# Kernel optimization log

Measured on AMD Instinct MI355X. Metric: run time of the kernel, lower is better.

## Reference

```python
import jax, jax.numpy as jnp
import numpy as np
import math

B, N, C = 8, 1024, 256
NUM_HEAD = 4
HEAD_DIM = C // NUM_HEAD
K_NN = 5
SAMPLE_RATIO = 0.25
CLUSTER_NUM = max(math.ceil(N * SAMPLE_RATIO), 1)
EPS = 1e-6


def cluster_dpc_knn(x, cluster_num, k):
    # DPC-KNN clustering (faithful to TCFormer's cluster_dpc_knn, run under no_grad in torch)
    b, n, c = x.shape
    sq = jnp.sum(x * x, axis=-1)
    d2 = sq[:, :, None] + sq[:, None, :] - 2.0 * jnp.einsum('bic,bjc->bij', x, x)
    dist = jnp.sqrt(jnp.maximum(d2, 0.0)) / jnp.sqrt(jnp.asarray(c, x.dtype))  # (b,n,n)
    # k smallest distances per token (includes self, dist 0)
    neg_near, _ = jax.lax.top_k(-dist, k)
    dist_nearest = -neg_near
    density = jnp.exp(-jnp.mean(dist_nearest ** 2, axis=-1))  # (b,n)
    # deterministic tiny noise for tie-breaking (torch adds rand*1e-6)
    density = density + jax.random.uniform(jax.random.key(42), density.shape, dtype=density.dtype) * 1e-6
    mask = (density[:, None, :] > density[:, :, None]).astype(x.dtype)
    dist_max = jnp.max(dist.reshape(b, -1), axis=-1)[:, None, None]
    d_ind = jnp.min(dist * mask + dist_max * (1.0 - mask), axis=-1)  # distance indicator
    score = d_ind * density
    _, index_down = jax.lax.top_k(score, cluster_num)  # (b,cluster_num) cluster centers
    dist_c = jnp.take_along_axis(dist, index_down[:, :, None], axis=1)  # (b,cn,n)
    idx_cluster = jnp.argmin(dist_c, axis=1)  # (b,n)
    # ensure each center maps to its own cluster id
    bidx = jnp.arange(b)[:, None]
    idx_cluster = idx_cluster.at[bidx, index_down].set(jnp.broadcast_to(jnp.arange(cluster_num)[None, :], (b, cluster_num)))
    return idx_cluster


def setup_inputs() -> dict:
    key = jax.random.key(0)
    ks = jax.random.split(key, 6)
    w_scale = 1.0 / jnp.sqrt(jnp.asarray(C, jnp.float32))
    x_token = jax.random.normal(ks[0], (B, N, C), dtype=jnp.float32)
    Wq = jax.random.normal(ks[1], (C, C), dtype=jnp.float32) * w_scale
    Wk = jax.random.normal(ks[2], (C, C), dtype=jnp.float32) * w_scale
    Wv = jax.random.normal(ks[3], (C, C), dtype=jnp.float32) * w_scale
    Wp = jax.random.normal(ks[4], (C, C), dtype=jnp.float32) * w_scale
    bp = jax.random.normal(ks[5], (C,), dtype=jnp.float32) * 0.01
    return {"x_token": x_token, "Wq": Wq, "Wk": Wk, "Wv": Wv, "Wp": Wp, "bp": bp}


def reference(x_token, Wq, Wk, Wv, Wp, bp):
    b, n, c = x_token.shape
    scale = HEAD_DIM ** -0.5
    idx_cluster = cluster_dpc_knn(x_token, CLUSTER_NUM, K_NN)  # (b,n) int
    q = (x_token @ Wq.T).reshape(b, n, NUM_HEAD, HEAD_DIM).transpose(0, 2, 1, 3)
    k = (x_token @ Wk.T).reshape(b, n, NUM_HEAD, HEAD_DIM).transpose(0, 2, 1, 3)
    v = (x_token @ Wv.T).reshape(b, n, NUM_HEAD, HEAD_DIM).transpose(0, 2, 1, 3)
    scores = jnp.einsum('bhid,bhjd->bhij', q, k) * scale  # (b,h,n,n)
    # scatter into (b,cluster_num,n,c) + sum over clusters == mask scores by same-cluster
    same = (idx_cluster[:, :, None] == idx_cluster[:, None, :])[:, None, :, :]
    attn = jnp.where(same, scores, 0.0)
    # original: masked_fill(attn == 0, -1e9) then exp in float32
    attn = jnp.where(attn == 0.0, -1e9, attn)
    attn = jnp.exp(attn.astype(jnp.float32))
    attn = (attn + EPS / n) / (jnp.sum(attn, axis=-1, keepdims=True) + EPS)
    out = jnp.einsum('bhij,bhjd->bhid', attn, v).transpose(0, 2, 1, 3).reshape(b, n, c)
    return out @ Wp.T + bp
```

## Files before the change

### kernel.cpp

```cpp
#include <hip/hip_runtime.h>
#include <math.h>

#define B_ 8
#define N_ 1024
#define C_ 256
#define H_ 4
#define D_ 64
#define CN_ 256
#define EPS_ 1e-6f

__device__ __forceinline__ unsigned rotl32(unsigned x, int r){ return (x<<r)|(x>>(32-r)); }

__device__ float tf_noise(unsigned gid){
  unsigned c0 = (gid >= 4096u) ? gid - 4096u : gid;
  unsigned c1 = c0 + 4096u;
  const unsigned k0 = 0u, k1 = 42u;
  const unsigned ks2 = k0 ^ k1 ^ 0x1BD11BDAu;
  unsigned x0 = c0 + k0, x1 = c1 + k1;
  const int R0[4] = {13,15,26,6};
  const int R1[4] = {17,29,16,24};
  #pragma unroll
  for (int i=0;i<4;i++){ x0 += x1; x1 = rotl32(x1,R0[i]); x1 ^= x0; }
  x0 += k1; x1 += ks2 + 1u;
  #pragma unroll
  for (int i=0;i<4;i++){ x0 += x1; x1 = rotl32(x1,R1[i]); x1 ^= x0; }
  x0 += ks2; x1 += k0 + 2u;
  #pragma unroll
  for (int i=0;i<4;i++){ x0 += x1; x1 = rotl32(x1,R0[i]); x1 ^= x0; }
  x0 += k0; x1 += k1 + 3u;
  #pragma unroll
  for (int i=0;i<4;i++){ x0 += x1; x1 = rotl32(x1,R1[i]); x1 ^= x0; }
  x0 += k1; x1 += ks2 + 4u;
  #pragma unroll
  for (int i=0;i<4;i++){ x0 += x1; x1 = rotl32(x1,R0[i]); x1 ^= x0; }
  x0 += ks2; x1 += k0 + 5u;
  unsigned bits = (gid >= 4096u) ? x1 : x0;
  return __uint_as_float(0x3F800000u | (bits >> 9)) - 1.0f;
}

__global__ __launch_bounds__(256) void k_sq(const float* __restrict__ x, float* __restrict__ sq){
  int row = blockIdx.x * 4 + (threadIdx.x >> 6);
  int l = threadIdx.x & 63;
  const float* p = x + (size_t)row * C_;
  float s = 0.f;
  #pragma unroll
  for (int t=0;t<4;t++){ float v = p[l + 64*t]; s += v*v; }
  #pragma unroll
  for (int m=32;m;m>>=1) s += __shfl_xor(s, m);
  if (l==0) sq[row] = s;
}

#define STAGE64(PA, PB)                                                        \
  _Pragma("unroll")                                                            \
  for (int f=0; f<4; f++){                                                     \
    int e = f*64 + t; int row = e >> 2, kq = e & 3;                            \
    float4 a = *(const float4*)(PA + (size_t)row*C_ + k0 + kq*4);              \
    float4 bq = *(const float4*)(PB + (size_t)row*C_ + k0 + kq*4);             \
    As[kq*4+0][row]=a.x;  As[kq*4+1][row]=a.y;                                 \
    As[kq*4+2][row]=a.z;  As[kq*4+3][row]=a.w;                                 \
    Bs[kq*4+0][row]=bq.x; Bs[kq*4+1][row]=bq.y;                                \
    Bs[kq*4+2][row]=bq.z; Bs[kq*4+3][row]=bq.w;                                \
  }

#define INNER64                                                                \
  _Pragma("unroll")                                                            \
  for (int kk=0;kk<16;kk++){                                                   \
    float4 a0 = *(const float4*)&As[kk][ty*4];                                 \
    float4 a1 = *(const float4*)&As[kk][32+ty*4];                              \
    float4 b0 = *(const float4*)&Bs[kk][tx*4];                                 \
    float4 b1 = *(const float4*)&Bs[kk][32+tx*4];                              \
    float av[8]={a0.x,a0.y,a0.z,a0.w,a1.x,a1.y,a1.z,a1.w};                     \
    float bv[8]={b0.x,b0.y,b0.z,b0.w,b1.x,b1.y,b1.z,b1.w};                     \
    _Pragma("unroll")                                                          \
    for (int r=0;r<8;r++)                                                      \
      _Pragma("unroll")                                                        \
      for (int c=0;c<8;c++) acc[r][c] += av[r]*bv[c];                          \
  }

__global__ __launch_bounds__(64) void k_dist3(const float* __restrict__ x, const float* __restrict__ sq,
                                              float* __restrict__ dist){
  int b = blockIdx.y;
  int p = blockIdx.x;
  int bi = 0, rem = p;
  while (rem >= 16 - bi){ rem -= 16 - bi; bi++; }
  int bj = bi + rem;
  const float* xb = x + (size_t)b*N_*C_;
  const float* pa = xb + (size_t)(bi*64)*C_;
  const float* pb = xb + (size_t)(bj*64)*C_;
  __shared__ float As[16][68];
  __shared__ float Bs[16][68];
  int t = threadIdx.x;
  int tx = t & 7, ty = t >> 3;
  float acc[8][8] = {};
  for (int k0=0; k0<C_; k0+=16){
    STAGE64(pa, pb)
    __syncthreads();
    INNER64
    __syncthreads();
  }
  float sqj[8];
  #pragma unroll
  for (int cc=0;cc<2;cc++)
    #pragma unroll
    for (int c=0;c<4;c++) sqj[cc*4+c] = sq[b*N_ + bj*64 + cc*32 + tx*4 + c];
  float o[8][8];
  #pragma unroll
  for (int rr=0;rr<2;rr++){
    #pragma unroll
    for (int r=0;r<4;r++){
      int i = bi*64 + rr*32 + ty*4 + r;
      float si = sq[b*N_ + i];
      #pragma unroll
      for (int cc=0;cc<2;cc++)
        #pragma unroll
        for (int c=0;c<4;c++){
          float d2 = si + sqj[cc*4+c] - 2.f*acc[rr*4+r][cc*4+c];
          o[rr*4+r][cc*4+c] = sqrtf(fmaxf(d2, 0.f)) * 0.0625f;
        }
    }
  }
  float* dbase = dist + (size_t)b*N_*N_;
  #pragma unroll
  for (int rr=0;rr<2;rr++)
    #pragma unroll
    for (int r=0;r<4;r++){
      int i = bi*64 + rr*32 + ty*4 + r;
      #pragma unroll
      for (int cc=0;cc<2;cc++){
        int j0 = bj*64 + cc*32 + tx*4;
        *(float4*)(dbase + (size_t)i*N_ + j0) =
          make_float4(o[rr*4+r][cc*4+0], o[rr*4+r][cc*4+1], o[rr*4+r][cc*4+2], o[rr*4+r][cc*4+3]);
      }
    }
  if (bi != bj){
    #pragma unroll
    for (int cc=0;cc<2;cc++)
      #pragma unroll
      for (int c=0;c<4;c++){
        int j = bj*64 + cc*32 + tx*4 + c;
        #pragma unroll
        for (int rr=0;rr<2;rr++){
          int i0 = bi*64 + rr*32 + ty*4;
          *(float4*)(dbase + (size_t)j*N_ + i0) =
            make_float4(o[rr*4+0][cc*4+c], o[rr*4+1][cc*4+c], o[rr*4+2][cc*4+c], o[rr*4+3][cc*4+c]);
        }
      }
  }
}

__global__ __launch_bounds__(64) void k_gemm3(const float* __restrict__ X,
    const float* __restrict__ W0, const float* __restrict__ W1, const float* __restrict__ W2,
    const float* __restrict__ bias,
    float* __restrict__ Y0, float* __restrict__ Y1, float* __restrict__ Y2){
  const float* W = (blockIdx.z==0)?W0:(blockIdx.z==1)?W1:W2;
  float* Y = (blockIdx.z==0)?Y0:(blockIdx.z==1)?Y1:Y2;
  int bi = blockIdx.y, bj = blockIdx.x;
  const float* pa = X + (size_t)(bi*64)*C_;
  const float* pb = W + (size_t)(bj*64)*C_;
  __shared__ float As[16][68];
  __shared__ float Bs[16][68];
  int t = threadIdx.x;
  int tx = t & 7, ty = t >> 3;
  float acc[8][8] = {};
  for (int k0=0; k0<C_; k0+=16){
    STAGE64(pa, pb)
    __syncthreads();
    INNER64
    __syncthreads();
  }
  float bs[8];
  #pragma unroll
  for (int cc=0;cc<2;cc++)
    #pragma unroll
    for (int c=0;c<4;c++) bs[cc*4+c] = bias ? bias[bj*64 + cc*32 + tx*4 + c] : 0.f;
  #pragma unroll
  for (int rr=0;rr<2;rr++)
    #pragma unroll
    for (int r=0;r<4;r++){
      int m = bi*64 + rr*32 + ty*4 + r;
      #pragma unroll
      for (int cc=0;cc<2;cc++){
        int j0 = bj*64 + cc*32 + tx*4;
        *(float4*)(Y + (size_t)m*C_ + j0) =
          make_float4(acc[rr*4+r][cc*4+0]+bs[cc*4+0], acc[rr*4+r][cc*4+1]+bs[cc*4+1],
                      acc[rr*4+r][cc*4+2]+bs[cc*4+2], acc[rr*4+r][cc*4+3]+bs[cc*4+3]);
      }
    }
}

__global__ __launch_bounds__(256) void k_top5(const float* __restrict__ dist, float* __restrict__ density,
                                              float* __restrict__ rowmax){
  int row = blockIdx.x * 4 + (threadIdx.x >> 6);
  int l = threadIdx.x & 63;
  const float* p = dist + (size_t)row * N_;
  float t[5] = {1e30f,1e30f,1e30f,1e30f,1e30f};
  float mx = 0.f;
  #pragma unroll
  for (int q2=0;q2<16;q2++){
    float v = p[l + 64*q2];
    mx = fmaxf(mx, v);
    if (v < t[4]){
      t[4] = v;
      #pragma unroll
      for (int a=4;a>0;a--) if (t[a] < t[a-1]) { float tmp=t[a]; t[a]=t[a-1]; t[a-1]=tmp; }
    }
  }
  #pragma unroll
  for (int m=32;m;m>>=1) mx = fmaxf(mx, __shfl_xor(mx, m));
  float sumsq = 0.f;
  int hi = 0;
  #pragma unroll
  for (int a=0;a<5;a++){
    float head = (hi==0)?t[0]:(hi==1)?t[1]:(hi==2)?t[2]:(hi==3)?t[3]:(hi==4)?t[4]:1e30f;
    float m = head;
    #pragma unroll
    for (int mm=32;mm;mm>>=1) m = fminf(m, __shfl_xor(m, mm));
    sumsq += m*m;
    unsigned long long ball = __ballot(head == m);
    if (l == (__ffsll(ball) - 1)) hi++;
  }
  if (l == 0){
    float msq = sumsq / 5.0f;
    density[row] = expf(-msq) + tf_noise((unsigned)row) * 1e-6f;
    rowmax[row] = mx;
  }
}

__global__ __launch_bounds__(256) void k_bmax(const float* __restrict__ rowmax, float* __restrict__ bmax){
  int b = blockIdx.x; int t = threadIdx.x;
  float m = fmaxf(fmaxf(rowmax[b*N_+t], rowmax[b*N_+t+256]),
                  fmaxf(rowmax[b*N_+t+512], rowmax[b*N_+t+768]));
  __shared__ float s[256];
  s[t]=m; __syncthreads();
  for (int d=128; d; d>>=1){ if (t<d) s[t]=fmaxf(s[t],s[t+d]); __syncthreads(); }
  if (t==0) bmax[b]=s[0];
}

__global__ __launch_bounds__(256) void k_dind(const float* __restrict__ dist, const float* __restrict__ density,
                                              const float* __restrict__ bmax, float* __restrict__ score){
  int row = blockIdx.x * 4 + (threadIdx.x >> 6);
  int b = row >> 10;
  int l = threadIdx.x & 63;
  const float* p = dist + (size_t)row * N_;
  const float* db = density + b*N_;
  float di = density[row];
  float m = bmax[b];
  #pragma unroll
  for (int q2=0;q2<16;q2++){
    int j = l + 64*q2;
    float dj = db[j];
    if (dj > di) m = fminf(m, p[j]);
  }
  #pragma unroll
  for (int mm=32;mm;mm>>=1) m = fminf(m, __shfl_xor(m, mm));
  if (l==0) score[row] = m * di;
}

__global__ __launch_bounds__(1024) void k_top256(const float* __restrict__ score, int* __restrict__ idxdown){
  int b = blockIdx.x; int t = threadIdx.x;
  __shared__ float sv[1024];
  __shared__ int si[1024];
  sv[t] = score[b*N_ + t]; si[t] = t;
  __syncthreads();
  for (int k = 2; k <= 1024; k <<= 1){
    for (int j = k >> 1; j > 0; j >>= 1){
      int l = t ^ j;
      if (l > t){
        bool up = ((t & k) == 0);
        float a = sv[t], b2 = sv[l]; int ai = si[t], bi2 = si[l];
        bool prec = (a > b2) || (a == b2 && ai < bi2);
        bool dosw = up ? (!prec) : prec;
        if (dosw){ sv[t]=b2; sv[l]=a; si[t]=bi2; si[l]=ai; }
      }
      __syncthreads();
    }
  }
  if (t < CN_) idxdown[b*CN_ + t] = si[t];
}

__global__ __launch_bounds__(256) void k_assign(const float* __restrict__ dist, const int* __restrict__ idxdown,
                                                int* __restrict__ idxclu){
  int b = blockIdx.y;
  int l = threadIdx.x & 63;
  int ch = threadIdx.x >> 6;
  int j = blockIdx.x*64 + l;
  __shared__ int cen[256];
  __shared__ float sd[4][64];
  __shared__ int sk[4][64];
  cen[threadIdx.x] = idxdown[b*CN_ + threadIdx.x];
  __syncthreads();
  const float* dbase = dist + (size_t)b*N_*N_;
  float best = 1e30f; int bk = 0;
  #pragma unroll 8
  for (int kk=0; kk<64; kk++){
    int k = ch*64 + kk;
    float d = dbase[(size_t)cen[k]*N_ + j];
    if (d < best){ best = d; bk = k; }
  }
  sd[ch][l] = best; sk[ch][l] = bk;
  __syncthreads();
  if (ch == 0){
    #pragma unroll
    for (int c2=1;c2<4;c2++){
      float d = sd[c2][l];
      if (d < best){ best = d; bk = sk[c2][l]; }
    }
    idxclu[b*N_ + j] = bk;
  }
}

__global__ void k_setcenters(const int* __restrict__ idxdown, int* __restrict__ idxclu){
  int b = blockIdx.x; int t = threadIdx.x;
  idxclu[b*N_ + idxdown[b*CN_ + t]] = t;
}

__global__ __launch_bounds__(256) void k_build(const int* __restrict__ idxclu, int* __restrict__ off,
                                               int* __restrict__ cnt, int* __restrict__ members){
  int b = blockIdx.x; int t = threadIdx.x;
  __shared__ int sc[256], so[256];
  sc[t] = 0;
  __syncthreads();
  int cl[4];
  #pragma unroll
  for (int i=0;i<4;i++){
    cl[i] = idxclu[b*N_ + i*256 + t];
    atomicAdd(&sc[cl[i]], 1);
  }
  __syncthreads();
  int mine = sc[t];
  so[t] = mine;
  __syncthreads();
  for (int d=1; d<256; d<<=1){
    int v2 = 0;
    if (t>=d) v2 = so[t-d];
    __syncthreads();
    if (t>=d) so[t] += v2;
    __syncthreads();
  }
  int excl = so[t] - mine;
  off[b*CN_+t] = excl;
  cnt[b*CN_+t] = mine;
  sc[t] = excl;
  __syncthreads();
  #pragma unroll
  for (int i=0;i<4;i++){
    int p = atomicAdd(&sc[cl[i]], 1);
    members[b*N_ + p] = i*256 + t;
  }
}

__global__ __launch_bounds__(256) void k_vsum1(const float* __restrict__ v, float* __restrict__ vsp){
  int p = blockIdx.x;
  int b = p >> 4, s = p & 15;
  int c = threadIdx.x;
  float acc = 0.f;
  const float* base = v + ((size_t)b*N_ + s*64)*C_ + c;
  #pragma unroll 8
  for (int i=0;i<64;i++) acc += base[(size_t)i*C_];
  vsp[(size_t)p*C_ + c] = acc;
}

__global__ __launch_bounds__(256) void k_vsum2(const float* __restrict__ vsp, float* __restrict__ vsum){
  int b = blockIdx.x; int c = threadIdx.x;
  float s = 0.f;
  #pragma unroll
  for (int i=0;i<16;i++) s += vsp[((size_t)b*16 + i)*C_ + c];
  vsum[b*C_ + c] = s;
}

__global__ __launch_bounds__(256) void k_attn(const float* __restrict__ q, const float* __restrict__ kmat,
                                              const float* __restrict__ v, const float* __restrict__ vsum,
                                              const int* __restrict__ idxclu, const int* __restrict__ off,
                                              const int* __restrict__ cnt, const int* __restrict__ members,
                                              float* __restrict__ att){
  int bi = blockIdx.x;
  int b = bi >> 10;
  int h = threadIdx.x >> 6, l = threadIdx.x & 63;
  int c = idxclu[bi];
  int o = off[b*CN_ + c], m = cnt[b*CN_ + c];
  int ch = h*64 + l;
  float qv = q[(size_t)bi*C_ + ch];
  float acc = 0.f, den = 0.f;
  const int* mem = members + b*N_ + o;
  for (int t=0;t<m;t++){
    int j = mem[t];
    size_t base = ((size_t)(b*N_ + j))*C_ + ch;
    float p = qv * kmat[base];
    #pragma unroll
    for (int mm=32;mm;mm>>=1) p += __shfl_xor(p, mm);
    float s = p * 0.125f;
    float e = (s == 0.0f) ? 0.0f : expf(s);
    den += e;
    acc += e * v[base];
  }
  float outv = (acc + (EPS_/1024.0f) * vsum[b*C_ + ch]) / (den + EPS_);
  att[(size_t)bi*C_ + ch] = outv;
}

extern "C" void kernel_launch(void* const* d_in, const int* in_sizes, int n_in,
                              void* d_out, int out_size, void* d_ws, size_t ws_size,
                              hipStream_t stream){
  const float* x  = (const float*)d_in[0];
  const float* Wq = (const float*)d_in[1];
  const float* Wk = (const float*)d_in[2];
  const float* Wv = (const float*)d_in[3];
  const float* Wp = (const float*)d_in[4];
  const float* bp = (const float*)d_in[5];
  float* out = (float*)d_out;

  float* ws = (float*)d_ws;
  float* dist    = ws;
  float* q       = dist + (size_t)B_*N_*N_;
  float* kk      = q    + (size_t)B_*N_*C_;
  float* v       = kk   + (size_t)B_*N_*C_;
  float* att     = v    + (size_t)B_*N_*C_;
  float* vsp     = att  + (size_t)B_*N_*C_;
  float* vsum    = vsp + 128*C_;
  float* sq      = vsum + B_*C_;
  float* rowmax  = sq + B_*N_;
  float* bmax    = rowmax + B_*N_;
  float* density = bmax + 16;
  float* score   = density + B_*N_;
  int* idxdown   = (int*)(score + B_*N_);
  int* idxclu    = idxdown + B_*CN_;
  int* cnt       = idxclu + B_*N_;
  int* off       = cnt + B_*CN_;
  int* members   = off + B_*CN_;

  k_sq<<<B_*N_/4,256,0,stream>>>(x, sq);
  k_dist3<<<dim3(136,8),64,0,stream>>>(x, sq, dist);
  k_top5<<<B_*N_/4,256,0,stream>>>(dist, density, rowmax);
  k_bmax<<<8,256,0,stream>>>(rowmax, bmax);
  k_dind<<<B_*N_/4,256,0,stream>>>(dist, density, bmax, score);
  k_top256<<<8,1024,0,stream>>>(score, idxdown);
  k_assign<<<dim3(16,8),256,0,stream>>>(dist, idxdown, idxclu);
  k_setcenters<<<8,256,0,stream>>>(idxdown, idxclu);
  k_build<<<8,256,0,stream>>>(idxclu, off, cnt, members);
  k_gemm3<<<dim3(4,128,3),64,0,stream>>>(x, Wq, Wk, Wv, nullptr, q, kk, v);
  k_vsum1<<<128,256,0,stream>>>(v, vsp);
  k_vsum2<<<8,256,0,stream>>>(vsp, vsum);
  k_attn<<<B_*N_,256,0,stream>>>(q, kk, v, vsum, idxclu, off, cnt, members, att);
  k_gemm3<<<dim3(4,128,1),64,0,stream>>>(att, Wp, Wp, Wp, bp, out, out, out);
}
```

Baseline: 307.1 us.

## Register-prefetch GEMM tiles and use wavefront shuffles in bitonic top-k

The shared FP32 GEMM loop used by the distance and QKV kernels now double-buffers global loads in registers, so the next K-slice is fetched while the current one is computed. Launch bounds are raised to request two blocks per CU. The bitonic sort for top-256 keeps each element in a register and uses __shfl_xor for strides under 64, going through shared memory only for larger strides. This cuts barrier and LDS traffic in the sort, at the cost of more registers in the GEMM kernels.

```diff
diff --git a/kernel.cpp b/kernel.cpp
--- a/kernel.cpp
+++ b/kernel.cpp
@@ -50,16 +50,22 @@
   if (l==0) sq[row] = s;
 }
 
-#define STAGE64(PA, PB)                                                        \
+#define GLOAD(RA, RB, PA, PB, K0)                                              \
   _Pragma("unroll")                                                            \
   for (int f=0; f<4; f++){                                                     \
     int e = f*64 + t; int row = e >> 2, kq = e & 3;                            \
-    float4 a = *(const float4*)(PA + (size_t)row*C_ + k0 + kq*4);              \
-    float4 bq = *(const float4*)(PB + (size_t)row*C_ + k0 + kq*4);             \
-    As[kq*4+0][row]=a.x;  As[kq*4+1][row]=a.y;                                 \
-    As[kq*4+2][row]=a.z;  As[kq*4+3][row]=a.w;                                 \
-    Bs[kq*4+0][row]=bq.x; Bs[kq*4+1][row]=bq.y;                                \
-    Bs[kq*4+2][row]=bq.z; Bs[kq*4+3][row]=bq.w;                                \
+    RA[f] = *(const float4*)(PA + (size_t)row*C_ + (K0) + kq*4);               \
+    RB[f] = *(const float4*)(PB + (size_t)row*C_ + (K0) + kq*4);               \
+  }
+
+#define LWRITE(RA, RB)                                                         \
+  _Pragma("unroll")                                                            \
+  for (int f=0; f<4; f++){                                                     \
+    int e = f*64 + t; int row = e >> 2, kq = e & 3;                            \
+    As[kq*4+0][row]=RA[f].x; As[kq*4+1][row]=RA[f].y;                          \
+    As[kq*4+2][row]=RA[f].z; As[kq*4+3][row]=RA[f].w;                          \
+    Bs[kq*4+0][row]=RB[f].x; Bs[kq*4+1][row]=RB[f].y;                          \
+    Bs[kq*4+2][row]=RB[f].z; Bs[kq*4+3][row]=RB[f].w;                          \
   }
 
 #define INNER64                                                                \
@@ -77,8 +83,24 @@
       for (int c=0;c<8;c++) acc[r][c] += av[r]*bv[c];                          \
   }
 
-__global__ __launch_bounds__(64) void k_dist3(const float* __restrict__ x, const float* __restrict__ sq,
-                                              float* __restrict__ dist){
+#define KLOOP_PIPE                                                             \
+  float4 rA0[4], rB0[4], rA1[4], rB1[4];                                       \
+  GLOAD(rA0, rB0, pa, pb, 0)                                                   \
+  for (int s2=0; s2<8; ++s2){                                                  \
+    LWRITE(rA0, rB0)                                                           \
+    __syncthreads();                                                           \
+    GLOAD(rA1, rB1, pa, pb, s2*32+16)                                          \
+    INNER64                                                                    \
+    __syncthreads();                                                           \
+    LWRITE(rA1, rB1)                                                           \
+    __syncthreads();                                                           \
+    if (s2<7){ GLOAD(rA0, rB0, pa, pb, s2*32+32) }                             \
+    INNER64                                                                    \
+    __syncthreads();                                                           \
+  }
+
+__global__ __launch_bounds__(64, 2) void k_dist3(const float* __restrict__ x, const float* __restrict__ sq,
+                                                 float* __restrict__ dist){
   int b = blockIdx.y;
   int p = blockIdx.x;
   int bi = 0, rem = p;
@@ -92,12 +114,7 @@
   int t = threadIdx.x;
   int tx = t & 7, ty = t >> 3;
   float acc[8][8] = {};
-  for (int k0=0; k0<C_; k0+=16){
-    STAGE64(pa, pb)
-    __syncthreads();
-    INNER64
-    __syncthreads();
-  }
+  KLOOP_PIPE
   float sqj[8];
   #pragma unroll
   for (int cc=0;cc<2;cc++)
@@ -148,7 +165,7 @@
   }
 }
 
-__global__ __launch_bounds__(64) void k_gemm3(const float* __restrict__ X,
+__global__ __launch_bounds__(64, 2) void k_gemm3(const float* __restrict__ X,
     const float* __restrict__ W0, const float* __restrict__ W1, const float* __restrict__ W2,
     const float* __restrict__ bias,
     float* __restrict__ Y0, float* __restrict__ Y1, float* __restrict__ Y2){
@@ -162,12 +179,7 @@
   int t = threadIdx.x;
   int tx = t & 7, ty = t >> 3;
   float acc[8][8] = {};
-  for (int k0=0; k0<C_; k0+=16){
-    STAGE64(pa, pb)
-    __syncthreads();
-    INNER64
-    __syncthreads();
-  }
+  KLOOP_PIPE
   float bs[8];
   #pragma unroll
   for (int cc=0;cc<2;cc++)
@@ -260,22 +272,30 @@
   int b = blockIdx.x; int t = threadIdx.x;
   __shared__ float sv[1024];
   __shared__ int si[1024];
-  sv[t] = score[b*N_ + t]; si[t] = t;
-  __syncthreads();
+  float v = score[b*N_ + t];
+  int i = t;
   for (int k = 2; k <= 1024; k <<= 1){
     for (int j = k >> 1; j > 0; j >>= 1){
-      int l = t ^ j;
-      if (l > t){
-        bool up = ((t & k) == 0);
-        float a = sv[t], b2 = sv[l]; int ai = si[t], bi2 = si[l];
-        bool prec = (a > b2) || (a == b2 && ai < bi2);
-        bool dosw = up ? (!prec) : prec;
-        if (dosw){ sv[t]=b2; sv[l]=a; si[t]=bi2; si[l]=ai; }
+      float v2; int i2;
+      if (j >= 64){
+        sv[t] = v; si[t] = i;
+        __syncthreads();
+        v2 = sv[t ^ j]; i2 = si[t ^ j];
+        __syncthreads();
+      } else {
+        v2 = __shfl_xor(v, j);
+        i2 = __shfl_xor(i, j);
       }
-      __syncthreads();
-    }
-  }
-  if (t < CN_) idxdown[b*CN_ + t] = si[t];
+      bool islo = (t & j) == 0;
+      float lov = islo ? v : v2,  hiv = islo ? v2 : v;
+      int   loi = islo ? i : i2,  hii = islo ? i2 : i;
+      bool prec = (lov > hiv) || (lov == hiv && loi < hii);
+      bool up = ((t & k) == 0);
+      bool dosw = up ? !prec : prec;
+      if (dosw){ v = v2; i = i2; }
+    }
+  }
+  if (t < CN_) idxdown[b*CN_ + t] = i;
 }
 
 __global__ __launch_bounds__(256) void k_assign(const float* __restrict__ dist, const int* __restrict__ idxdown,
```

After: 712.8 us. +132.1%, slower.
